# Performance work log

Hardware: AMD Instinct MI355X
Metric: run time of the kernel (lower is better)

Reference implementation:

```python
import jax, jax.numpy as jnp
import numpy as np
from jax.scipy.special import gammaln

N_I = 100000
N_J = 100000
D = 8
S_I = 6000
S_J = 6000
NNZ = 500000
EPS = 1e-06


def setup_inputs() -> dict:
    key = jax.random.key(0)
    ks = jax.random.split(key, 9)
    beta = jax.random.normal(ks[0], (N_I,), dtype=jnp.float32)
    gamma = jax.random.normal(ks[1], (N_J,), dtype=jnp.float32)
    latent_zi = jax.random.normal(ks[2], (N_I, D), dtype=jnp.float32)
    latent_zj = jax.random.normal(ks[3], (N_J, D), dtype=jnp.float32)
    # multinomial-without-replacement node samples -> random permutation prefix
    sample_i_idx = jax.random.permutation(ks[4], N_I)[:S_I]
    sample_j_idx = jax.random.permutation(ks[5], N_J)[:S_J]
    # spspmm-selected subgraph links (global node indices) with edge counts
    sparse_i_sample = jax.random.randint(ks[6], (NNZ,), 0, N_I)
    sparse_j_sample = jax.random.randint(ks[7], (NNZ,), 0, N_J)
    valueC = jax.random.uniform(ks[8], (NNZ,), dtype=jnp.float32)
    return {
        'beta': beta, 'gamma': gamma,
        'latent_zi': latent_zi, 'latent_zj': latent_zj,
        'valueC': valueC,
        'sample_i_idx': sample_i_idx, 'sample_j_idx': sample_j_idx,
        'sparse_i_sample': sparse_i_sample, 'sparse_j_sample': sparse_j_sample,
    }


def reference(beta, gamma, latent_zi, latent_zj, valueC,
              sample_i_idx, sample_j_idx, sparse_i_sample, sparse_j_sample):
    # Dense non-link term over sampled (I, J) block
    zi = latent_zi[sample_i_idx]            # [S_I, D]
    zj = latent_zj[sample_j_idx]            # [S_J, D]
    diff = zi[:, None, :] - zj[None, :, :] + EPS   # [S_I, S_J, D]
    z_dist = jnp.sqrt(jnp.sum(diff * diff, axis=-1))  # [S_I, S_J]
    Lambda = beta[sample_i_idx][:, None] + gamma[sample_j_idx][None, :] - z_dist
    # Sparse link terms (Poisson log-likelihood)
    dl = latent_zi[sparse_i_sample] - latent_zj[sparse_j_sample] + EPS  # [NNZ, D]
    z_dist_links = jnp.sqrt(jnp.sum(dl * dl, axis=-1))                  # [NNZ]
    bias_links = beta[sparse_i_sample] + gamma[sparse_j_sample]
    log_Lambda_links = valueC * (bias_links - z_dist_links)
    LL = jnp.sum(log_Lambda_links - gammaln(valueC + 1.0)) - jnp.sum(jnp.exp(Lambda))
    return LL
```

## Files before the change

### kernel.cpp

```cpp
#include <hip/hip_runtime.h>
#include <hip/hip_fp16.h>
#include <math.h>

#define NI_TOT 100000
#define NJ_TOT 100000
#define DD 8
#define SI_N 6000
#define SJ_N 6000
#define NNZ_N 500000
#define EPSF 1e-6f
#define LOG2E 1.44269504088896f

#define TI 64
#define JPT 2
#define JTILE (256 * JPT)
#define ND_I ((SI_N + TI - 1) / TI)
#define NJT ((SJ_N + JTILE - 1) / JTILE)
#define N_DENSE_BLOCKS (ND_I * NJT)
#define LPT 2
#define SPARSE_SPAN (256 * LPT)
#define N_SPARSE_BLOCKS ((NNZ_N + SPARSE_SPAN - 1) / SPARSE_SPAN)
#define N_TOTAL_BLOCKS (N_DENSE_BLOCKS + N_SPARSE_BLOCKS)

#define NROWS (NI_TOT + NJ_TOT)
#define HZ_BYTES ((size_t)NROWS * DD * 2)
#define HB_BYTES ((size_t)NROWS * 2)
#define PARTIALS_OFF (HZ_BYTES + HB_BYTES)

#define GA1 (-0.577191652f)
#define GA2 ( 0.988205891f)
#define GA3 (-0.897056937f)
#define GA4 ( 0.918206857f)
#define GA5 (-0.756704078f)
#define GA6 ( 0.482199394f)
#define GA7 (-0.193527818f)
#define GA8 ( 0.035868343f)

__global__ __launch_bounds__(256) void pack_kernel(
    const float* __restrict__ beta, const float* __restrict__ gamma,
    const float* __restrict__ zi_all, const float* __restrict__ zj_all,
    __half* __restrict__ hz, __half* __restrict__ hb)
{
    const int r = blockIdx.x * 256 + threadIdx.x;
    if (r < NROWS) {
        const float* src = (r < NI_TOT) ? zi_all + (size_t)r * DD
                                        : zj_all + (size_t)(r - NI_TOT) * DD;
        float4 a = ((const float4*)src)[0];
        float4 b = ((const float4*)src)[1];
        __half2 h0 = __floats2half2_rn(a.x, a.y);
        __half2 h1 = __floats2half2_rn(a.z, a.w);
        __half2 h2 = __floats2half2_rn(b.x, b.y);
        __half2 h3 = __floats2half2_rn(b.z, b.w);
        uint4 u;
        u.x = *(unsigned*)&h0; u.y = *(unsigned*)&h1;
        u.z = *(unsigned*)&h2; u.w = *(unsigned*)&h3;
        ((uint4*)hz)[r] = u;
    } else if (r < 2 * NROWS) {
        const int q = r - NROWS;
        float v = (q < NI_TOT) ? beta[q] : gamma[q - NI_TOT];
        hb[q] = __float2half(v);
    }
}

__device__ __forceinline__ void unpack_row(uint4 u, float f[DD]) {
    float2 p;
    p = __half22float2(*(__half2*)&u.x); f[0] = p.x; f[1] = p.y;
    p = __half22float2(*(__half2*)&u.y); f[2] = p.x; f[3] = p.y;
    p = __half22float2(*(__half2*)&u.z); f[4] = p.x; f[5] = p.y;
    p = __half22float2(*(__half2*)&u.w); f[6] = p.x; f[7] = p.y;
}

__global__ __launch_bounds__(256) void fused_kernel(
    const float* __restrict__ beta, const float* __restrict__ gamma,
    const float* __restrict__ zi_all, const float* __restrict__ zj_all,
    const float* __restrict__ valueC,
    const int* __restrict__ si, const int* __restrict__ sj,
    const int* __restrict__ spi, const int* __restrict__ spj,
    const __half* __restrict__ hz, const __half* __restrict__ hb,
    float* __restrict__ partials, float* __restrict__ out, int mode)
{
    __shared__ float sRed[4];
    const int t = threadIdx.x;

    float blocksum = 0.0f;

    if (blockIdx.x < N_DENSE_BLOCKS) {
        __shared__ __align__(16) float  sZi[TI * DD];
        __shared__ __align__(8)  float2 sIB[TI];

        const int it = blockIdx.x % ND_I;
        const int js = blockIdx.x / ND_I;
        const int i0 = it * TI;

        for (int idx = t; idx < TI * DD; idx += 256) {
            int r = idx >> 3, d = idx & 7;
            int gi = i0 + r;
            float v = (gi < SI_N) ? zi_all[(size_t)si[gi] * DD + d] : 0.0f;
            sZi[idx] = (v + EPSF) * LOG2E;
        }
        __syncthreads();
        if (t < TI) {
            int gi = i0 + t;
            float s = 0.0f;
#pragma unroll
            for (int d = 0; d < DD; ++d) {
                float v = sZi[t * DD + d];
                s = fmaf(v, v, s);
            }
            float bL = (gi < SI_N) ? beta[si[gi]] * LOG2E : -1e30f;
            sIB[t] = make_float2(s, bL);
        }

        const int jb = js * JTILE + t * JPT;
        float zA[DD], zB[DD], glA, glB, s2A, s2B;
        {
            int gj = jb;
            if (gj < SJ_N) {
                int row = sj[gj];
                const float4* q = (const float4*)(zj_all + (size_t)row * DD);
                float4 q0 = q[0], q1 = q[1];
                zA[0]=q0.x*LOG2E; zA[1]=q0.y*LOG2E; zA[2]=q0.z*LOG2E; zA[3]=q0.w*LOG2E;
                zA[4]=q1.x*LOG2E; zA[5]=q1.y*LOG2E; zA[6]=q1.z*LOG2E; zA[7]=q1.w*LOG2E;
                glA = gamma[row] * LOG2E;
            } else {
#pragma unroll
                for (int d = 0; d < DD; ++d) zA[d] = 0.0f;
                glA = -1e30f;
            }
            gj = jb + 1;
            if (gj < SJ_N) {
                int row = sj[gj];
                const float4* q = (const float4*)(zj_all + (size_t)row * DD);
                float4 q0 = q[0], q1 = q[1];
                zB[0]=q0.x*LOG2E; zB[1]=q0.y*LOG2E; zB[2]=q0.z*LOG2E; zB[3]=q0.w*LOG2E;
                zB[4]=q1.x*LOG2E; zB[5]=q1.y*LOG2E; zB[6]=q1.z*LOG2E; zB[7]=q1.w*LOG2E;
                glB = gamma[row] * LOG2E;
            } else {
#pragma unroll
                for (int d = 0; d < DD; ++d) zB[d] = 0.0f;
                glB = -1e30f;
            }
            float sa = 0.0f, sb = 0.0f;
#pragma unroll
            for (int d = 0; d < DD; ++d) {
                sa = fmaf(zA[d], zA[d], sa);
                sb = fmaf(zB[d], zB[d], sb);
            }
            s2A = sa; s2B = sb;
        }
        __syncthreads();

        float acc0 = 0.0f, acc1 = 0.0f;
        float4 cr0 = *(const float4*)&sZi[0];
        float4 cr1 = *(const float4*)&sZi[4];
        float2 cib = sIB[0];
#pragma unroll 4
        for (int a = 0; a < TI; ++a) {
            float4 nr0, nr1; float2 nib;
            if (a + 1 < TI) {
                nr0 = *(const float4*)&sZi[(a + 1) * DD];
                nr1 = *(const float4*)&sZi[(a + 1) * DD + 4];
                nib = sIB[a + 1];
            }
            float dA = 0.0f, dB = 0.0f;
            dA = fmaf(cr0.x, zA[0], dA); dB = fmaf(cr0.x, zB[0], dB);
            dA = fmaf(cr0.y, zA[1], dA); dB = fmaf(cr0.y, zB[1], dB);
            dA = fmaf(cr0.z, zA[2], dA); dB = fmaf(cr0.z, zB[2], dB);
            dA = fmaf(cr0.w, zA[3], dA); dB = fmaf(cr0.w, zB[3], dB);
            dA = fmaf(cr1.x, zA[4], dA); dB = fmaf(cr1.x, zB[4], dB);
            dA = fmaf(cr1.y, zA[5], dA); dB = fmaf(cr1.y, zB[5], dB);
            dA = fmaf(cr1.z, zA[6], dA); dB = fmaf(cr1.z, zB[6], dB);
            dA = fmaf(cr1.w, zA[7], dA); dB = fmaf(cr1.w, zB[7], dB);
            float ssA = fmaf(dA, -2.0f, cib.x + s2A);
            float ssB = fmaf(dB, -2.0f, cib.x + s2B);
            ssA = fmaxf(ssA, 1e-20f);
            ssB = fmaxf(ssB, 1e-20f);
            float xA = cib.y + glA - __builtin_amdgcn_sqrtf(ssA);
            float xB = cib.y + glB - __builtin_amdgcn_sqrtf(ssB);
            acc0 += __builtin_amdgcn_exp2f(xA);
            acc1 += __builtin_amdgcn_exp2f(xB);
            cr0 = nr0; cr1 = nr1; cib = nib;
        }
        blocksum = -(acc0 + acc1);
    } else {
        const int base = (blockIdx.x - N_DENSE_BLOCKS) * SPARSE_SPAN + t;
        float val = 0.0f;
        const uint4* hzv = (const uint4*)hz;
#pragma unroll
        for (int u = 0; u < LPT; ++u) {
            const int idx = base + u * 256;
            if (idx >= NNZ_N) continue;
            const int i = spi[idx], j = spj[idx];
            const float c = valueC[idx];
            float dist, bg;
            if (mode == 0) {
                uint4 ui = hzv[i];
                uint4 uj = hzv[NI_TOT + j];
                float fi[DD], fj[DD];
                unpack_row(ui, fi);
                unpack_row(uj, fj);
                float ss = 0.0f;
#pragma unroll
                for (int d = 0; d < DD; ++d) {
                    float df = fi[d] - fj[d] + EPSF;
                    ss = fmaf(df, df, ss);
                }
                ss = fmaxf(ss, 1e-20f);
                dist = __builtin_amdgcn_sqrtf(ss);
                bg = __half2float(hb[i]) + __half2float(hb[NI_TOT + j]);
            } else {
                const float4* zi4 = (const float4*)(zi_all + (size_t)i * DD);
                const float4* zj4 = (const float4*)(zj_all + (size_t)j * DD);
                float4 a0 = zi4[0], a1 = zi4[1];
                float4 b0 = zj4[0], b1 = zj4[1];
                float ss = 0.0f, df;
                df = a0.x-b0.x+EPSF; ss = fmaf(df,df,ss);
                df = a0.y-b0.y+EPSF; ss = fmaf(df,df,ss);
                df = a0.z-b0.z+EPSF; ss = fmaf(df,df,ss);
                df = a0.w-b0.w+EPSF; ss = fmaf(df,df,ss);
                df = a1.x-b1.x+EPSF; ss = fmaf(df,df,ss);
                df = a1.y-b1.y+EPSF; ss = fmaf(df,df,ss);
                df = a1.z-b1.z+EPSF; ss = fmaf(df,df,ss);
                df = a1.w-b1.w+EPSF; ss = fmaf(df,df,ss);
                ss = fmaxf(ss, 1e-20f);
                dist = __builtin_amdgcn_sqrtf(ss);
                bg = beta[i] + gamma[j];
            }
            float g = 1.0f + c*(GA1 + c*(GA2 + c*(GA3 + c*(GA4 + c*(GA5
                          + c*(GA6 + c*(GA7 + c*GA8)))))));
            val += c * (bg - dist) - __builtin_amdgcn_logf(g) * (1.0f / LOG2E);
        }
        blocksum = val;
    }

    float acc = blocksum;
#pragma unroll
    for (int off = 32; off; off >>= 1) acc += __shfl_down(acc, off, 64);
    const int lane = t & 63, w = t >> 6;
    if (lane == 0) sRed[w] = acc;
    __syncthreads();
    if (t == 0) {
        float s = sRed[0] + sRed[1] + sRed[2] + sRed[3];
        if (mode) atomicAdd(out, s);
        else partials[blockIdx.x] = s;
    }
}

__global__ __launch_bounds__(256) void final_reduce_kernel(
    const float* __restrict__ p, int n, float* __restrict__ out)
{
    __shared__ float sRed[4];
    float s0 = 0.0f, s1 = 0.0f, s2 = 0.0f, s3 = 0.0f;
    int i = threadIdx.x;
    for (; i + 768 < n; i += 1024) {
        s0 += p[i]; s1 += p[i + 256]; s2 += p[i + 512]; s3 += p[i + 768];
    }
    for (; i < n; i += 256) s0 += p[i];
    float s = (s0 + s1) + (s2 + s3);
#pragma unroll
    for (int off = 32; off; off >>= 1) s += __shfl_down(s, off, 64);
    const int lane = threadIdx.x & 63, w = threadIdx.x >> 6;
    if (lane == 0) sRed[w] = s;
    __syncthreads();
    if (threadIdx.x == 0) out[0] = sRed[0] + sRed[1] + sRed[2] + sRed[3];
}

extern "C" void kernel_launch(void* const* d_in, const int* in_sizes, int n_in,
                              void* d_out, int out_size, void* d_ws, size_t ws_size,
                              hipStream_t stream) {
    const float* beta   = (const float*)d_in[0];
    const float* gamma  = (const float*)d_in[1];
    const float* zi     = (const float*)d_in[2];
    const float* zj     = (const float*)d_in[3];
    const float* valueC = (const float*)d_in[4];
    const int* si   = (const int*)d_in[5];
    const int* sjx  = (const int*)d_in[6];
    const int* spi  = (const int*)d_in[7];
    const int* spj  = (const int*)d_in[8];
    float* out = (float*)d_out;

    const int ntot = N_TOTAL_BLOCKS;
    const size_t need = PARTIALS_OFF + (size_t)ntot * sizeof(float);

    if (ws_size >= need) {
        __half* hz = (__half*)d_ws;
        __half* hb = (__half*)((char*)d_ws + HZ_BYTES);
        float* p = (float*)((char*)d_ws + PARTIALS_OFF);
        const int packb = (2 * NROWS + 255) / 256;
        pack_kernel<<<packb, 256, 0, stream>>>(beta, gamma, zi, zj, hz, hb);
        fused_kernel<<<ntot, 256, 0, stream>>>(
            beta, gamma, zi, zj, valueC, si, sjx, spi, spj, hz, hb, p, out, 0);
        final_reduce_kernel<<<1, 256, 0, stream>>>(p, ntot, out);
    } else {
        hipMemsetAsync(out, 0, sizeof(float), stream);
        fused_kernel<<<ntot, 256, 0, stream>>>(
            beta, gamma, zi, zj, valueC, si, sjx, spi, spj,
            (const __half*)zi, (const __half*)zi, nullptr, out, 1);
    }
}
```

Before: 110.9 us.

## Fold final reduction into fused kernel via last-block counter; double sparse links per thread

Removes the separate final_reduce kernel launch. Each block writes its partial, increments an agent-scope atomic counter, and the last block to arrive sums all partials. The counter is reset inside pack_kernel. LPT also goes from 2 to 4, halving the number of sparse blocks and giving each thread more links to process. This saves one launch and its gap, at the cost of a fence and an atomic in every block.

Measured after the change: 174.1 us. 57.0% more time.

```diff
diff --git a/kernel.cpp b/kernel.cpp
--- a/kernel.cpp
+++ b/kernel.cpp
@@ -17,7 +17,7 @@
 #define ND_I ((SI_N + TI - 1) / TI)
 #define NJT ((SJ_N + JTILE - 1) / JTILE)
 #define N_DENSE_BLOCKS (ND_I * NJT)
-#define LPT 2
+#define LPT 4
 #define SPARSE_SPAN (256 * LPT)
 #define N_SPARSE_BLOCKS ((NNZ_N + SPARSE_SPAN - 1) / SPARSE_SPAN)
 #define N_TOTAL_BLOCKS (N_DENSE_BLOCKS + N_SPARSE_BLOCKS)
@@ -26,6 +26,7 @@
 #define HZ_BYTES ((size_t)NROWS * DD * 2)
 #define HB_BYTES ((size_t)NROWS * 2)
 #define PARTIALS_OFF (HZ_BYTES + HB_BYTES)
+#define COUNTER_OFF (PARTIALS_OFF + (size_t)N_TOTAL_BLOCKS * 4)
 
 #define GA1 (-0.577191652f)
 #define GA2 ( 0.988205891f)
@@ -39,9 +40,11 @@
 __global__ __launch_bounds__(256) void pack_kernel(
     const float* __restrict__ beta, const float* __restrict__ gamma,
     const float* __restrict__ zi_all, const float* __restrict__ zj_all,
-    __half* __restrict__ hz, __half* __restrict__ hb)
+    __half* __restrict__ hz, __half* __restrict__ hb,
+    unsigned* __restrict__ counter)
 {
     const int r = blockIdx.x * 256 + threadIdx.x;
+    if (r == 0) *counter = 0u;
     if (r < NROWS) {
         const float* src = (r < NI_TOT) ? zi_all + (size_t)r * DD
                                         : zj_all + (size_t)(r - NI_TOT) * DD;
@@ -77,9 +80,11 @@
     const int* __restrict__ si, const int* __restrict__ sj,
     const int* __restrict__ spi, const int* __restrict__ spj,
     const __half* __restrict__ hz, const __half* __restrict__ hb,
-    float* __restrict__ partials, float* __restrict__ out, int mode)
+    float* __restrict__ partials, unsigned* __restrict__ counter,
+    float* __restrict__ out, int mode)
 {
     __shared__ float sRed[4];
+    __shared__ int sLast;
     const int t = threadIdx.x;
 
     float blocksum = 0.0f;
@@ -239,30 +244,31 @@
     const int lane = t & 63, w = t >> 6;
     if (lane == 0) sRed[w] = acc;
     __syncthreads();
+
+    if (mode) {
+        if (t == 0) atomicAdd(out, sRed[0] + sRed[1] + sRed[2] + sRed[3]);
+        return;
+    }
+
     if (t == 0) {
-        float s = sRed[0] + sRed[1] + sRed[2] + sRed[3];
-        if (mode) atomicAdd(out, s);
-        else partials[blockIdx.x] = s;
-    }
-}
-
-__global__ __launch_bounds__(256) void final_reduce_kernel(
-    const float* __restrict__ p, int n, float* __restrict__ out)
-{
-    __shared__ float sRed[4];
-    float s0 = 0.0f, s1 = 0.0f, s2 = 0.0f, s3 = 0.0f;
-    int i = threadIdx.x;
-    for (; i + 768 < n; i += 1024) {
-        s0 += p[i]; s1 += p[i + 256]; s2 += p[i + 512]; s3 += p[i + 768];
-    }
-    for (; i < n; i += 256) s0 += p[i];
-    float s = (s0 + s1) + (s2 + s3);
-#pragma unroll
-    for (int off = 32; off; off >>= 1) s += __shfl_down(s, off, 64);
-    const int lane = threadIdx.x & 63, w = threadIdx.x >> 6;
-    if (lane == 0) sRed[w] = s;
+        partials[blockIdx.x] = sRed[0] + sRed[1] + sRed[2] + sRed[3];
+        __threadfence();
+        unsigned old = __hip_atomic_fetch_add(counter, 1u, __ATOMIC_ACQ_REL,
+                                              __HIP_MEMORY_SCOPE_AGENT);
+        sLast = (old == gridDim.x - 1);
+    }
     __syncthreads();
-    if (threadIdx.x == 0) out[0] = sRed[0] + sRed[1] + sRed[2] + sRed[3];
+    if (sLast) {
+        float s = 0.0f;
+        for (int i = t; i < (int)gridDim.x; i += 256)
+            s += __hip_atomic_load(&partials[i], __ATOMIC_RELAXED,
+                                   __HIP_MEMORY_SCOPE_AGENT);
+#pragma unroll
+        for (int off = 32; off; off >>= 1) s += __shfl_down(s, off, 64);
+        if (lane == 0) sRed[w] = s;
+        __syncthreads();
+        if (t == 0) out[0] = sRed[0] + sRed[1] + sRed[2] + sRed[3];
+    }
 }
 
 extern "C" void kernel_launch(void* const* d_in, const int* in_sizes, int n_in,
@@ -280,21 +286,22 @@
     float* out = (float*)d_out;
 
     const int ntot = N_TOTAL_BLOCKS;
-    const size_t need = PARTIALS_OFF + (size_t)ntot * sizeof(float);
+    const size_t need = COUNTER_OFF + 4;
 
     if (ws_size >= need) {
         __half* hz = (__half*)d_ws;
         __half* hb = (__half*)((char*)d_ws + HZ_BYTES);
-        float* p = (float*)((char*)d_ws + PARTIALS_OFF);
+        float* p   = (float*)((char*)d_ws + PARTIALS_OFF);
+        unsigned* counter = (unsigned*)((char*)d_ws + COUNTER_OFF);
         const int packb = (2 * NROWS + 255) / 256;
-        pack_kernel<<<packb, 256, 0, stream>>>(beta, gamma, zi, zj, hz, hb);
+        pack_kernel<<<packb, 256, 0, stream>>>(beta, gamma, zi, zj, hz, hb, counter);
         fused_kernel<<<ntot, 256, 0, stream>>>(
-            beta, gamma, zi, zj, valueC, si, sjx, spi, spj, hz, hb, p, out, 0);
-        final_reduce_kernel<<<1, 256, 0, stream>>>(p, ntot, out);
+            beta, gamma, zi, zj, valueC, si, sjx, spi, spj, hz, hb,
+            p, counter, out, 0);
     } else {
         hipMemsetAsync(out, 0, sizeof(float), stream);
         fused_kernel<<<ntot, 256, 0, stream>>>(
             beta, gamma, zi, zj, valueC, si, sjx, spi, spj,
-            (const __half*)zi, (const __half*)zi, nullptr, out, 1);
+            (const __half*)zi, (const __half*)zi, nullptr, nullptr, out, 1);
     }
 }
```
